# Optimization experiments

Hardware: AMD Instinct MI355X
Metric: run time of the kernel (lower is better)

## Reference

```python
import jax, jax.numpy as jnp
import numpy as np

N_QUBITS = 5
DIM = 2 ** N_QUBITS  # 32
B = 262144

# PauliZ eigenvalue signs per basis state per wire (wire 0 = most significant bit)
_SIGNS = np.stack(
    [1.0 - 2.0 * ((np.arange(DIM) >> (N_QUBITS - 1 - q)) & 1) for q in range(N_QUBITS)],
    axis=1,
).astype(np.float32)  # (DIM, N_QUBITS)


def _cnot_perm(ctrl, tgt):
    # CNOT is a basis permutation: flip target bit where control bit is 1.
    pos_c = N_QUBITS - 1 - ctrl
    pos_t = N_QUBITS - 1 - tgt
    idx = np.arange(DIM)
    cbit = (idx >> pos_c) & 1
    return idx ^ (cbit << pos_t)


def _apply_1q(state, gate, q):
    # state: (B, DIM) complex64; gate: (2,2) shared or (B,2,2) batched
    b = state.shape[0]
    s = state.reshape(b, 2 ** q, 2, 2 ** (N_QUBITS - 1 - q))
    if gate.ndim == 3:
        s = jnp.einsum('bij,bajk->baik', gate, s)
    else:
        s = jnp.einsum('ij,bajk->baik', gate, s)
    return s.reshape(b, DIM)


def _rx_gates(theta):
    # RX(theta) per sample: theta (B,) -> (B,2,2) complex64
    c = jnp.cos(theta * 0.5).astype(jnp.complex64)
    s = (-1j) * jnp.sin(theta * 0.5).astype(jnp.complex64)
    return jnp.stack([jnp.stack([c, s], -1), jnp.stack([s, c], -1)], -2)


def _rot_gate(phi, theta, omega):
    # PennyLane Rot(phi, theta, omega) = RZ(omega) @ RY(theta) @ RZ(phi)
    c = jnp.cos(theta * 0.5)
    s = jnp.sin(theta * 0.5)
    e = lambda a: jnp.exp(1j * a)
    g00 = e(-(phi + omega) * 0.5) * c
    g01 = -e((phi - omega) * 0.5) * s
    g10 = e(-(phi - omega) * 0.5) * s
    g11 = e((phi + omega) * 0.5) * c
    return jnp.stack([jnp.stack([g00, g01]), jnp.stack([g10, g11])]).astype(jnp.complex64)


def _simulate(x, w):
    b = x.shape[0]
    state = jnp.zeros((b, DIM), jnp.complex64).at[:, 0].set(1.0)
    # AngleEmbedding (default rotation='X'): RX(x[:, q]) on wire q
    for q in range(N_QUBITS):
        state = _apply_1q(state, _rx_gates(x[:, q]), q)
    # StronglyEntanglingLayers: per layer, Rot on every wire then ring of CNOTs
    n_layers = w.shape[0]
    for l in range(n_layers):
        for q in range(N_QUBITS):
            state = _apply_1q(state, _rot_gate(w[l, q, 0], w[l, q, 1], w[l, q, 2]), q)
        r = (l % (N_QUBITS - 1)) + 1  # default ranges in PennyLane
        for q in range(N_QUBITS):
            perm = _cnot_perm(q, (q + r) % N_QUBITS)
            state = state[:, perm]
    return state


def setup_inputs() -> dict:
    key = jax.random.key(0)
    k1, k2, k3, k4 = jax.random.split(key, 4)
    return {
        'x': jax.random.normal(k1, (B, N_QUBITS), jnp.float32),
        'w': jax.random.normal(k2, (2, N_QUBITS, 3), jnp.float32),
        'fc_w': jax.random.normal(k3, (8, N_QUBITS), jnp.float32),
        'fc_b': jax.random.normal(k4, (8,), jnp.float32),
    }


def reference(x, w, fc_w, fc_b):
    state = _simulate(x, w)                      # (B, 32) complex64
    probs = state.real ** 2 + state.imag ** 2    # (B, 32)
    expvals = probs @ jnp.asarray(_SIGNS)        # (B, 5) PauliZ expectations
    return expvals @ fc_w.T + fc_b               # (B, 8)
```

## Files before the change

### kernel.cpp

```cpp
#include <hip/hip_runtime.h>

typedef float f2 __attribute__((ext_vector_type(2)));

#define N_QUBITS 5
#define DIM 32

__host__ __device__ constexpr int cnot_apply(int i, int ctrl, int tgt) {
    const int pc = N_QUBITS - 1 - ctrl;
    const int pt = N_QUBITS - 1 - tgt;
    return i ^ (((i >> pc) & 1) << pt);
}
__host__ __device__ constexpr int layer_perm(int i, int r) {
    int idx = i;
    for (int q = N_QUBITS - 1; q >= 0; --q)
        idx = cnot_apply(idx, q, (q + r) % N_QUBITS);
    return idx;
}
__host__ __device__ constexpr int invP1(int p) {
    for (int l = 0; l < 32; ++l) if (layer_perm(l, 1) == p) return l;
    return 0;
}

__global__ __launch_bounds__(256, 2) void vqc_kernel(
    const float* __restrict__ x,
    const float* __restrict__ w,
    const float* __restrict__ fc_w,
    const float* __restrict__ fc_b,
    float* __restrict__ out,
    int Btot)
{
    __shared__ float s_g0[N_QUBITS][8];
    __shared__ float s_cs[N_QUBITS][2];
    __shared__ f2    s_ph[DIM];
    __shared__ float s_fc_w[40];
    __shared__ float s_fc_b[8];

    const int t = threadIdx.x;
    if (t < N_QUBITS) {
        const float phi = w[t * 3 + 0];
        const float th  = w[t * 3 + 1];
        const float om  = w[t * 3 + 2];
        float s, c;   sincosf(0.5f * th, &s, &c);
        float sp, cp; sincosf(0.5f * (phi + om), &sp, &cp);
        float sm, cm; sincosf(0.5f * (phi - om), &sm, &cm);
        s_g0[t][0] =  cp * c;  s_g0[t][1] = -sp * c;
        s_g0[t][2] = -cm * s;  s_g0[t][3] = -sm * s;
        s_g0[t][4] =  cm * s;  s_g0[t][5] = -sm * s;
        s_g0[t][6] =  cp * c;  s_g0[t][7] =  sp * c;
    } else if (t >= 8 && t < 13) {
        const int q = t - 8;
        float s, c;
        sincosf(0.5f * w[(N_QUBITS + q) * 3 + 1], &s, &c);
        s_cs[q][0] = c;  s_cs[q][1] = s;
    } else if (t >= 32 && t < 64) {
        const int j = t - 32;
        const int i = invP1(j);
        float ang = 0.f;
#pragma unroll
        for (int q = 0; q < N_QUBITS; ++q) {
            const float ph = w[(N_QUBITS + q) * 3 + 0];
            ang += ((i >> (4 - q)) & 1) ? 0.5f * ph : -0.5f * ph;
        }
        float s, c;
        sincosf(ang, &s, &c);
        s_ph[j] = f2{c, s};
    } else if (t >= 64 && t < 104) {
        s_fc_w[t - 64] = fc_w[t - 64];
    } else if (t >= 104 && t < 112) {
        s_fc_b[t - 104] = fc_b[t - 104];
    }
    __syncthreads();

    const int b0 = blockIdx.x * 512 + t;
    if (b0 >= Btot) return;
    const int b1 = b0 + 256;
    const int b1c = (b1 < Btot) ? b1 : b0;

    const float* xp0 = x + (size_t)b0 * 5;
    const float* xp1 = x + (size_t)b1c * 5;

    f2 sre[DIM], sim[DIM];
    {
        float s0, c0, s1, c1;
        __sincosf(0.5f * xp0[0], &s0, &c0);
        __sincosf(0.5f * xp1[0], &s1, &c1);
        const f2 cc = f2{c0, c1}, ss = f2{s0, s1};
        sre[0]  = s_g0[0][0] * cc + s_g0[0][3] * ss;
        sim[0]  = s_g0[0][1] * cc - s_g0[0][2] * ss;
        sre[16] = s_g0[0][4] * cc + s_g0[0][7] * ss;
        sim[16] = s_g0[0][5] * cc - s_g0[0][6] * ss;
    }
#pragma unroll
    for (int q = 1; q < N_QUBITS; ++q) {
        float s0, c0, s1, c1;
        __sincosf(0.5f * xp0[q], &s0, &c0);
        __sincosf(0.5f * xp1[q], &s1, &c1);
        const f2 cc = f2{c0, c1}, ss = f2{s0, s1};
        const f2 v0re = s_g0[q][0] * cc + s_g0[q][3] * ss;
        const f2 v0im = s_g0[q][1] * cc - s_g0[q][2] * ss;
        const f2 v1re = s_g0[q][4] * cc + s_g0[q][7] * ss;
        const f2 v1im = s_g0[q][5] * cc - s_g0[q][6] * ss;
        const int stride = 1 << (4 - q);
#pragma unroll
        for (int k = 0; k < (1 << q); ++k) {
            const int m = k * (stride << 1);
            const f2 are = sre[m], aim = sim[m];
            sre[m + stride] = v1re * are - v1im * aim;
            sim[m + stride] = v1re * aim + v1im * are;
            sre[m]          = v0re * are - v0im * aim;
            sim[m]          = v0re * aim + v0im * are;
        }
    }

#pragma unroll
    for (int j = 0; j < DIM; ++j) {
        const f2 ph = s_ph[j];
        const f2 re = sre[j], im = sim[j];
        sre[j] = re * ph.x - im * ph.y;
        sim[j] = re * ph.y + im * ph.x;
    }

#pragma unroll
    for (int q = 0; q < N_QUBITS; ++q) {
        const float c = s_cs[q][0], s = s_cs[q][1];
        const int stride = 1 << (4 - q);
        const int mask = stride - 1;
#pragma unroll
        for (int p = 0; p < DIM / 2; ++p) {
            const int a0 = ((p & ~mask) << 1) | (p & mask);
            const int ia = layer_perm(a0, 1);
            const int ib = layer_perm(a0 + stride, 1);
            const f2 ar = sre[ia], ai = sim[ia];
            const f2 br = sre[ib], bi = sim[ib];
            sre[ia] = c * ar - s * br;
            sim[ia] = c * ai - s * bi;
            sre[ib] = s * ar + c * br;
            sim[ib] = s * ai + c * bi;
        }
    }

    f2 pr[DIM];
#pragma unroll
    for (int i = 0; i < DIM; ++i) {
        const int j = layer_perm(layer_perm(i, 2), 1);
        pr[i] = sre[j] * sre[j] + sim[j] * sim[j];
    }

    f2 v16[16], v8_[8], v4_[4], v2_[2];
    f2 ev4 = f2{0.f, 0.f}, ev3 = f2{0.f, 0.f}, ev2 = f2{0.f, 0.f}, ev1 = f2{0.f, 0.f};
#pragma unroll
    for (int j = 0; j < 16; ++j) { v16[j] = pr[2*j] + pr[2*j+1]; ev4 += pr[2*j] - pr[2*j+1]; }
#pragma unroll
    for (int j = 0; j < 8; ++j)  { v8_[j] = v16[2*j] + v16[2*j+1]; ev3 += v16[2*j] - v16[2*j+1]; }
#pragma unroll
    for (int j = 0; j < 4; ++j)  { v4_[j] = v8_[2*j] + v8_[2*j+1]; ev2 += v8_[2*j] - v8_[2*j+1]; }
#pragma unroll
    for (int j = 0; j < 2; ++j)  { v2_[j] = v4_[2*j] + v4_[2*j+1]; ev1 += v4_[2*j] - v4_[2*j+1]; }
    const f2 ev0 = v2_[0] - v2_[1];
    const f2 ev[N_QUBITS] = {ev0, ev1, ev2, ev3, ev4};

    f2 o[8];
#pragma unroll
    for (int j = 0; j < 8; ++j) {
        f2 acc = f2{s_fc_b[j], s_fc_b[j]};
#pragma unroll
        for (int q = 0; q < 5; ++q) acc += ev[q] * s_fc_w[j * 5 + q];
        o[j] = acc;
    }

    float4* op0 = (float4*)(out + (size_t)b0 * 8);
    op0[0] = make_float4(o[0].x, o[1].x, o[2].x, o[3].x);
    op0[1] = make_float4(o[4].x, o[5].x, o[6].x, o[7].x);
    if (b1 < Btot) {
        float4* op1 = (float4*)(out + (size_t)b1 * 8);
        op1[0] = make_float4(o[0].y, o[1].y, o[2].y, o[3].y);
        op1[1] = make_float4(o[4].y, o[5].y, o[6].y, o[7].y);
    }
}

extern "C" void kernel_launch(void* const* d_in, const int* in_sizes, int n_in,
                              void* d_out, int out_size, void* d_ws, size_t ws_size,
                              hipStream_t stream) {
    const float* x    = (const float*)d_in[0];
    const float* w    = (const float*)d_in[1];
    const float* fc_w = (const float*)d_in[2];
    const float* fc_b = (const float*)d_in[3];
    float* out = (float*)d_out;

    const int Btot = in_sizes[0] / N_QUBITS;
    const int grid = (Btot + 511) / 512;
    hipLaunchKernelGGL(vqc_kernel, dim3(grid), dim3(256), 0, stream,
                       x, w, fc_w, fc_b, out, Btot);
}
```

Measured before the change: 14.91 us.

## Replace statevector simulation with Heisenberg-picture Pauli expansion of expectations

Replaces the 32-amplitude statevector evolution of the second layer and the probability reduction with a closed-form Pauli expansion. The first layer yields a product state whose per-qubit Bloch components (EZ, EX, EY) are computed directly. Each final PauliZ observable is back-propagated through the CNOT ring and the second-layer rotations at compile time into a sum of Pauli-string products, evaluated with templates. This removes the large register arrays and most FLOPs, and launch bounds are raised to allow more waves per CU. The risk is that the compile-time sign and permutation bookkeeping must exactly match the circuit's CNOT ordering.

```diff
diff --git a/kernel.cpp b/kernel.cpp
--- a/kernel.cpp
+++ b/kernel.cpp
@@ -16,12 +16,107 @@
         idx = cnot_apply(idx, q, (q + r) % N_QUBITS);
     return idx;
 }
-__host__ __device__ constexpr int invP1(int p) {
-    for (int l = 0; l < 32; ++l) if (layer_perm(l, 1) == p) return l;
+__host__ __device__ constexpr int invP(int p, int r) {
+    for (int l = 0; l < 32; ++l) if (layer_perm(l, r) == p) return l;
     return 0;
 }
-
-__global__ __launch_bounds__(256, 2) void vqc_kernel(
+__host__ __device__ constexpr int pc5(int m) {
+    int c = 0;
+    for (int b = 0; b < 5; ++b) c += (m >> b) & 1;
+    return c;
+}
+__host__ __device__ constexpr int pow3(int n) {
+    int r = 1;
+    for (int i = 0; i < n; ++i) r *= 3;
+    return r;
+}
+__host__ __device__ constexpr int Mmask(int q) {
+    int m = 0;
+    for (int b = 0; b < 5; ++b)
+        m |= ((invP(1 << b, 2) >> (4 - q)) & 1) << b;
+    return m;
+}
+__host__ __device__ constexpr int NC(int q) { return pow3(pc5(Mmask(q))); }
+
+struct SInfo {
+    int sign;
+    int nf;
+    int fidx[5];
+    int k;
+    int eb[5];
+    int et[5];
+};
+
+__host__ __device__ constexpr SInfo make_sinfo(int Q, int C) {
+    SInfo s{};
+    const int M = Mmask(Q);
+    int x = 0, z = 0, c = C;
+    s.nf = 0;
+    for (int b = 0; b < 5; ++b) {
+        if ((M >> b) & 1) {
+            const int t = c % 3; c /= 3;
+            s.fidx[s.nf] = b * 3 + t;
+            s.nf++;
+            if (t == 0)      z |= 1 << b;
+            else if (t == 1) x |= 1 << b;
+            else           { x |= 1 << b; z |= 1 << b; }
+        }
+    }
+    const int xp = layer_perm(x, 1);
+    int zp = 0;
+    for (int b = 0; b < 5; ++b)
+        zp |= (pc5(z & invP(1 << b, 1)) & 1) << b;
+    const int d  = pc5(x & z) - pc5(xp & zp);
+    const int dm = ((d % 4) + 4) % 4;
+    s.sign = (dm == 0) ? 1 : -1;
+    s.k = 0;
+    for (int b = 0; b < 5; ++b) {
+        const int tx = (xp >> b) & 1, tz = (zp >> b) & 1;
+        if (tx | tz) {
+            s.eb[s.k] = b;
+            s.et[s.k] = tx ? (tz ? 2 : 1) : 0;
+            s.k++;
+        }
+    }
+    return s;
+}
+
+#define EPICK(T, B) ((T) == 0 ? EZ[B] : ((T) == 1 ? EX[B] : EY[B]))
+
+template<int Q, int C>
+__device__ __forceinline__ f2 sterm(const float (&a)[15],
+        const f2 (&EZ)[5], const f2 (&EX)[5], const f2 (&EY)[5]) {
+    constexpr SInfo s = make_sinfo(Q, C);
+    float cf = a[s.fidx[0]];
+    if constexpr (s.nf > 1) cf *= a[s.fidx[1]];
+    if constexpr (s.nf > 2) cf *= a[s.fidx[2]];
+    if constexpr (s.nf > 3) cf *= a[s.fidx[3]];
+    if constexpr (s.nf > 4) cf *= a[s.fidx[4]];
+    f2 e = EPICK(s.et[0], s.eb[0]);
+    if constexpr (s.k > 1) e = e * EPICK(s.et[1], s.eb[1]);
+    if constexpr (s.k > 2) e = e * EPICK(s.et[2], s.eb[2]);
+    if constexpr (s.k > 3) e = e * EPICK(s.et[3], s.eb[3]);
+    if constexpr (s.k > 4) e = e * EPICK(s.et[4], s.eb[4]);
+    if constexpr (s.sign < 0) return e * (-cf);
+    else                      return e * cf;
+}
+
+template<int Q, int C>
+struct SSum {
+    static __device__ __forceinline__ f2 go(const float (&a)[15],
+            const f2 (&EZ)[5], const f2 (&EX)[5], const f2 (&EY)[5]) {
+        return SSum<Q, C - 1>::go(a, EZ, EX, EY) + sterm<Q, C>(a, EZ, EX, EY);
+    }
+};
+template<int Q>
+struct SSum<Q, 0> {
+    static __device__ __forceinline__ f2 go(const float (&a)[15],
+            const f2 (&EZ)[5], const f2 (&EX)[5], const f2 (&EY)[5]) {
+        return sterm<Q, 0>(a, EZ, EX, EY);
+    }
+};
+
+__global__ __launch_bounds__(256, 4) void vqc_kernel(
     const float* __restrict__ x,
     const float* __restrict__ w,
     const float* __restrict__ fc_w,
@@ -30,8 +125,7 @@
     int Btot)
 {
     __shared__ float s_g0[N_QUBITS][8];
-    __shared__ float s_cs[N_QUBITS][2];
-    __shared__ f2    s_ph[DIM];
+    __shared__ float s_a[15];
     __shared__ float s_fc_w[40];
     __shared__ float s_fc_b[8];
 
@@ -49,21 +143,14 @@
         s_g0[t][6] =  cp * c;  s_g0[t][7] =  sp * c;
     } else if (t >= 8 && t < 13) {
         const int q = t - 8;
-        float s, c;
-        sincosf(0.5f * w[(N_QUBITS + q) * 3 + 1], &s, &c);
-        s_cs[q][0] = c;  s_cs[q][1] = s;
-    } else if (t >= 32 && t < 64) {
-        const int j = t - 32;
-        const int i = invP1(j);
-        float ang = 0.f;
-#pragma unroll
-        for (int q = 0; q < N_QUBITS; ++q) {
-            const float ph = w[(N_QUBITS + q) * 3 + 0];
-            ang += ((i >> (4 - q)) & 1) ? 0.5f * ph : -0.5f * ph;
-        }
-        float s, c;
-        sincosf(ang, &s, &c);
-        s_ph[j] = f2{c, s};
+        const float phi = w[(N_QUBITS + q) * 3 + 0];
+        const float th  = w[(N_QUBITS + q) * 3 + 1];
+        float sth, cth; sincosf(th,  &sth, &cth);
+        float sph, cph; sincosf(phi, &sph, &cph);
+        const int b = 4 - q;
+        s_a[b * 3 + 0] = cth;
+        s_a[b * 3 + 1] = -sth * cph;
+        s_a[b * 3 + 2] =  sth * sph;
     } else if (t >= 64 && t < 104) {
         s_fc_w[t - 64] = fc_w[t - 64];
     } else if (t >= 104 && t < 112) {
@@ -79,19 +166,9 @@
     const float* xp0 = x + (size_t)b0 * 5;
     const float* xp1 = x + (size_t)b1c * 5;
 
-    f2 sre[DIM], sim[DIM];
-    {
-        float s0, c0, s1, c1;
-        __sincosf(0.5f * xp0[0], &s0, &c0);
-        __sincosf(0.5f * xp1[0], &s1, &c1);
-        const f2 cc = f2{c0, c1}, ss = f2{s0, s1};
-        sre[0]  = s_g0[0][0] * cc + s_g0[0][3] * ss;
-        sim[0]  = s_g0[0][1] * cc - s_g0[0][2] * ss;
-        sre[16] = s_g0[0][4] * cc + s_g0[0][7] * ss;
-        sim[16] = s_g0[0][5] * cc - s_g0[0][6] * ss;
-    }
-#pragma unroll
-    for (int q = 1; q < N_QUBITS; ++q) {
+    f2 EZ[5], EX[5], EY[5];
+#pragma unroll
+    for (int q = 0; q < N_QUBITS; ++q) {
         float s0, c0, s1, c1;
         __sincosf(0.5f * xp0[q], &s0, &c0);
         __sincosf(0.5f * xp1[q], &s1, &c1);
@@ -100,64 +177,22 @@
         const f2 v0im = s_g0[q][1] * cc - s_g0[q][2] * ss;
         const f2 v1re = s_g0[q][4] * cc + s_g0[q][7] * ss;
         const f2 v1im = s_g0[q][5] * cc - s_g0[q][6] * ss;
-        const int stride = 1 << (4 - q);
-#pragma unroll
-        for (int k = 0; k < (1 << q); ++k) {
-            const int m = k * (stride << 1);
-            const f2 are = sre[m], aim = sim[m];
-            sre[m + stride] = v1re * are - v1im * aim;
-            sim[m + stride] = v1re * aim + v1im * are;
-            sre[m]          = v0re * are - v0im * aim;
-            sim[m]          = v0re * aim + v0im * are;
-        }
-    }
-
-#pragma unroll
-    for (int j = 0; j < DIM; ++j) {
-        const f2 ph = s_ph[j];
-        const f2 re = sre[j], im = sim[j];
-        sre[j] = re * ph.x - im * ph.y;
-        sim[j] = re * ph.y + im * ph.x;
-    }
-
-#pragma unroll
-    for (int q = 0; q < N_QUBITS; ++q) {
-        const float c = s_cs[q][0], s = s_cs[q][1];
-        const int stride = 1 << (4 - q);
-        const int mask = stride - 1;
-#pragma unroll
-        for (int p = 0; p < DIM / 2; ++p) {
-            const int a0 = ((p & ~mask) << 1) | (p & mask);
-            const int ia = layer_perm(a0, 1);
-            const int ib = layer_perm(a0 + stride, 1);
-            const f2 ar = sre[ia], ai = sim[ia];
-            const f2 br = sre[ib], bi = sim[ib];
-            sre[ia] = c * ar - s * br;
-            sim[ia] = c * ai - s * bi;
-            sre[ib] = s * ar + c * br;
-            sim[ib] = s * ai + c * bi;
-        }
-    }
-
-    f2 pr[DIM];
-#pragma unroll
-    for (int i = 0; i < DIM; ++i) {
-        const int j = layer_perm(layer_perm(i, 2), 1);
-        pr[i] = sre[j] * sre[j] + sim[j] * sim[j];
-    }
-
-    f2 v16[16], v8_[8], v4_[4], v2_[2];
-    f2 ev4 = f2{0.f, 0.f}, ev3 = f2{0.f, 0.f}, ev2 = f2{0.f, 0.f}, ev1 = f2{0.f, 0.f};
-#pragma unroll
-    for (int j = 0; j < 16; ++j) { v16[j] = pr[2*j] + pr[2*j+1]; ev4 += pr[2*j] - pr[2*j+1]; }
-#pragma unroll
-    for (int j = 0; j < 8; ++j)  { v8_[j] = v16[2*j] + v16[2*j+1]; ev3 += v16[2*j] - v16[2*j+1]; }
-#pragma unroll
-    for (int j = 0; j < 4; ++j)  { v4_[j] = v8_[2*j] + v8_[2*j+1]; ev2 += v8_[2*j] - v8_[2*j+1]; }
-#pragma unroll
-    for (int j = 0; j < 2; ++j)  { v2_[j] = v4_[2*j] + v4_[2*j+1]; ev1 += v4_[2*j] - v4_[2*j+1]; }
-    const f2 ev0 = v2_[0] - v2_[1];
-    const f2 ev[N_QUBITS] = {ev0, ev1, ev2, ev3, ev4};
+        const int b = 4 - q;
+        EZ[b] = v0re * v0re + v0im * v0im - v1re * v1re - v1im * v1im;
+        EX[b] = 2.f * (v0re * v1re + v0im * v1im);
+        EY[b] = 2.f * (v0re * v1im - v0im * v1re);
+    }
+
+    float a[15];
+#pragma unroll
+    for (int i = 0; i < 15; ++i) a[i] = s_a[i];
+
+    f2 ev[N_QUBITS];
+    ev[0] = SSum<0, NC(0) - 1>::go(a, EZ, EX, EY);
+    ev[1] = SSum<1, NC(1) - 1>::go(a, EZ, EX, EY);
+    ev[2] = SSum<2, NC(2) - 1>::go(a, EZ, EX, EY);
+    ev[3] = SSum<3, NC(3) - 1>::go(a, EZ, EX, EY);
+    ev[4] = SSum<4, NC(4) - 1>::go(a, EZ, EX, EY);
 
     f2 o[8];
 #pragma unroll
```

Result: faster. 14.33 us (-3.9%).
